# Kernel tuning notes

Measured on AMD Instinct MI355X. Metric: run time of the kernel, lower is better.

The kernel has to match this reference:

```python
import jax, jax.numpy as jnp
import numpy as np

S, DIM, H, HD, RATIO = 1024, 1024, 16, 64, 4
EH = H * RATIO  # expanded heads = 64


def setup_inputs() -> dict:
    key = jax.random.key(0)
    ks = jax.random.split(key, 9)
    sc = 0.02
    return {
        "x": jax.random.normal(ks[0], (S, DIM), jnp.float32),
        "qkv_w": jax.random.normal(ks[1], (3 * DIM, DIM), jnp.float32) * sc,
        "qkv_b": jnp.zeros((3 * DIM,), jnp.float32),
        "proj_w": jax.random.normal(ks[2], (DIM, DIM), jnp.float32) * sc,
        "proj_b": jnp.zeros((DIM,), jnp.float32),
        "ap1_w": jax.random.normal(ks[3], (EH, H), jnp.float32) * 0.25,
        "ap1_b": jnp.zeros((EH,), jnp.float32),
        "ap2_w": jax.random.normal(ks[4], (H, EH), jnp.float32) * 0.125,
        "ap2_b": jnp.zeros((H,), jnp.float32),
    }


def reference(x, qkv_w, qkv_b, proj_w, proj_b, ap1_w, ap1_b, ap2_w, ap2_b):
    # qkv projection: s, 3*dim -> (3, h, s, d)
    qkv = x @ qkv_w.T + qkv_b
    qkv = qkv.reshape(S, 3, H, HD).transpose(1, 2, 0, 3)
    q, k, v = qkv[0], qkv[1], qkv[2]  # each [h, s, d]

    # scaled QK^T scores [h, q, k]
    attn = jnp.einsum("hqd,hkd->hqk", q, k) / jnp.sqrt(jnp.float32(HD))

    # talking-heads pre-softmax mix over head axis: [h,q,k] -> [e,q,k]
    attn = jnp.einsum("hqk,eh->eqk", attn, ap1_w) + ap1_b[:, None, None]

    # softmax over key axis (original: softmax axis=1 on 'q k h' layout)
    attn = jax.nn.softmax(attn, axis=2)

    # talking-heads post-softmax mix back: [e,q,k] -> [h,q,k]
    attn = jnp.einsum("eqk,he->hqk", attn, ap2_w) + ap2_b[:, None, None]

    # attn @ V, merge heads, output projection
    out = jnp.einsum("hqk,hkd->hqd", attn, v)
    out = out.transpose(1, 0, 2).reshape(S, DIM)
    return out @ proj_w.T + proj_b
```

## Files before the change

### kernel.cpp

```cpp
#include <hip/hip_runtime.h>
#include <hip/hip_bf16.h>
#include <cstdint>

#define S_LEN 1024
#define DIM   1024
#define NH    16
#define HD    64
#define EH    64

typedef __attribute__((ext_vector_type(8))) short short8v;
typedef __attribute__((ext_vector_type(4))) float f32x4;

static __device__ __forceinline__ short f2bf(float f) {
  union { float f; uint32_t u; } v; v.f = f;
  const uint32_t r = v.u + 0x7FFF + ((v.u >> 16) & 1);
  return (short)(r >> 16);
}
static __device__ __forceinline__ uint32_t packbf(float a, float b) {
  return (uint32_t)(uint16_t)f2bf(a) | ((uint32_t)(uint16_t)f2bf(b) << 16);
}

__global__ __launch_bounds__(256) void prep(
    const float* __restrict__ x, const float* __restrict__ qw,
    const float* __restrict__ pw, const float* __restrict__ proj_b,
    short* __restrict__ xb, short* __restrict__ wqb, short* __restrict__ wpb,
    float* __restrict__ out)
{
  const int i = blockIdx.x * 256 + threadIdx.x;
  if (i < 655360) {
    const float* s; short* d; int j = i;
    if (j < 131072)       { s = x;  d = xb; }
    else if (j < 524288)  { j -= 131072; s = qw; d = wqb; }
    else                  { j -= 524288; s = pw; d = wpb; }
    const float4 a = ((const float4*)s)[2 * j];
    const float4 b = ((const float4*)s)[2 * j + 1];
    short8v o;
    o[0] = f2bf(a.x); o[1] = f2bf(a.y); o[2] = f2bf(a.z); o[3] = f2bf(a.w);
    o[4] = f2bf(b.x); o[5] = f2bf(b.y); o[6] = f2bf(b.z); o[7] = f2bf(b.w);
    *(short8v*)(d + 8 * (size_t)j) = o;
  } else {
    const int j = i - 655360;
    ((float4*)out)[j] = ((const float4*)proj_b)[j & 255];
  }
}

__global__ __launch_bounds__(256) void transpose_v(
    const short* __restrict__ qkvb, short* __restrict__ Vt)
{
  const int h  = blockIdx.y;
  const int k0 = blockIdx.x * 32;
  const int d  = threadIdx.x & 63;
  const int kw = threadIdx.x >> 6;
  const short* src = qkvb + 2048 + h * 64 + d;
  short8v o;
  #pragma unroll
  for (int j = 0; j < 8; ++j)
    o[j] = src[(size_t)(k0 + kw * 8 + j) * 3072];
  *(short8v*)(Vt + ((size_t)h * 64 + d) * 1024 + k0 + kw * 8) = o;
}

template<int BM, int NSPLIT, int CMODE>
__global__ __launch_bounds__(256) void gemm_v2(
    const short* __restrict__ A, int lda, long long aStride,
    const short* __restrict__ B, int ldb, long long bStride,
    void* __restrict__ C_, int ldc, long long cStride,
    int K, float alpha, const float* __restrict__ bias)
{
  constexpr int MS = BM / 32;
  __shared__ short As[BM * 64];
  __shared__ short Bs[64 * 64];

  const int z = blockIdx.z, batch = z / NSPLIT, split = z % NSPLIT;
  A += (size_t)batch * aStride;
  B += (size_t)batch * bStride;

  const int t = threadIdx.x, wid = t >> 6, lane = t & 63;
  const int wr = wid >> 1, wc = wid & 1;
  const int fr = lane & 15, kg = lane >> 4;
  const int m0 = blockIdx.y * BM, n0 = blockIdx.x * 64;
  const int klen = K / NSPLIT, kbeg = split * klen;

  f32x4 acc[MS][2] = {};

  for (int k0 = kbeg; k0 < kbeg + klen; k0 += 64) {
    #pragma unroll
    for (int i = 0; i < BM / 32; ++i) {
      const int p = t + i * 256;
      const int row = p >> 3, pc = p & 7;
      *(short8v*)&As[row * 64 + ((pc ^ (row & 7)) << 3)] =
          *(const short8v*)(A + (size_t)(m0 + row) * lda + k0 + pc * 8);
    }
    #pragma unroll
    for (int i = 0; i < 2; ++i) {
      const int p = t + i * 256;
      const int row = p >> 3, pc = p & 7;
      *(short8v*)&Bs[row * 64 + ((pc ^ (row & 7)) << 3)] =
          *(const short8v*)(B + (size_t)(n0 + row) * ldb + k0 + pc * 8);
    }
    __syncthreads();

    #pragma unroll
    for (int sub = 0; sub < 2; ++sub) {
      short8v af[MS], bg[2];
      #pragma unroll
      for (int ms = 0; ms < MS; ++ms) {
        const int row = wr * (BM / 2) + ms * 16 + fr;
        af[ms] = *(const short8v*)&As[row * 64 + (((sub * 4 + kg) ^ (row & 7)) << 3)];
      }
      #pragma unroll
      for (int ns = 0; ns < 2; ++ns) {
        const int row = wc * 32 + ns * 16 + fr;
        bg[ns] = *(const short8v*)&Bs[row * 64 + (((sub * 4 + kg) ^ (row & 7)) << 3)];
      }
      #pragma unroll
      for (int ms = 0; ms < MS; ++ms)
        #pragma unroll
        for (int ns = 0; ns < 2; ++ns)
          acc[ms][ns] = __builtin_amdgcn_mfma_f32_16x16x32_bf16(
              af[ms], bg[ns], acc[ms][ns], 0, 0, 0);
    }
    __syncthreads();
  }

  #pragma unroll
  for (int ms = 0; ms < MS; ++ms) {
    #pragma unroll
    for (int ns = 0; ns < 2; ++ns) {
      const int col = n0 + wc * 32 + ns * 16 + fr;
      const float bv = (CMODE == 0 && bias) ? bias[col] : 0.f;
      #pragma unroll
      for (int j = 0; j < 4; ++j) {
        const int row = m0 + wr * (BM / 2) + ms * 16 + kg * 4 + j;
        const float val = acc[ms][ns][j] * alpha + bv;
        const size_t off = (size_t)batch * cStride + (size_t)row * ldc + col;
        if constexpr (CMODE == 0) ((short*)C_)[off] = f2bf(val);
        else                      atomicAdd((float*)C_ + off, val);
      }
    }
  }
}

__global__ __launch_bounds__(256) void scores_direct(
    const short* __restrict__ qkvb, short* __restrict__ Sb)
{
  const int h = blockIdx.z;
  const int t = threadIdx.x, wid = t >> 6, lane = t & 63;
  const int wr = wid >> 1, wc = wid & 1;
  const int fr = lane & 15, kg = lane >> 4;
  const int m0 = blockIdx.y * 128, n0 = blockIdx.x * 64;

  const short* Aq = qkvb + h * 64;
  const short* Bk = qkvb + 1024 + h * 64;

  f32x4 acc[4][2] = {};
  #pragma unroll
  for (int sub = 0; sub < 2; ++sub) {
    const int d8 = (sub * 4 + kg) * 8;
    short8v af[4], bg[2];
    #pragma unroll
    for (int ms = 0; ms < 4; ++ms)
      af[ms] = *(const short8v*)(Aq + (size_t)(m0 + wr * 64 + ms * 16 + fr) * 3072 + d8);
    #pragma unroll
    for (int ns = 0; ns < 2; ++ns)
      bg[ns] = *(const short8v*)(Bk + (size_t)(n0 + wc * 32 + ns * 16 + fr) * 3072 + d8);
    #pragma unroll
    for (int ms = 0; ms < 4; ++ms)
      #pragma unroll
      for (int ns = 0; ns < 2; ++ns)
        acc[ms][ns] = __builtin_amdgcn_mfma_f32_16x16x32_bf16(
            af[ms], bg[ns], acc[ms][ns], 0, 0, 0);
  }

  short* Ch = Sb + ((size_t)h << 20);
  #pragma unroll
  for (int ms = 0; ms < 4; ++ms)
    #pragma unroll
    for (int ns = 0; ns < 2; ++ns) {
      const int col = n0 + wc * 32 + ns * 16 + fr;
      #pragma unroll
      for (int j = 0; j < 4; ++j) {
        const int row = m0 + wr * 64 + ms * 16 + kg * 4 + j;
        Ch[(size_t)row * 1024 + col] = f2bf(acc[ms][ns][j] * 0.125f);
      }
    }
}

__global__ __launch_bounds__(256, 3) void mix_softmax(
    short* __restrict__ Sb,
    const float* __restrict__ ap1_w,
    const float* __restrict__ ap2_w,
    const float* __restrict__ ap2_b)
{
  __shared__ short St[S_LEN][16];
  __shared__ short Pt[4][16][72];
  __shared__ float red[4][EH];
  __shared__ float il_tab[EH];

  const int q = blockIdx.x, t = threadIdx.x;
  const int w = t >> 6, lane = t & 63, kg = lane >> 4, fr = lane & 15;
  const size_t qoff = (size_t)q << 10;

  for (int i = t; i < 1024; i += 256) {
    const int hp = i & 7, k8 = (i >> 3) * 8;
    const short8v v0 = *(const short8v*)(Sb + ((size_t)(2 * hp)     << 20) + qoff + k8);
    const short8v v1 = *(const short8v*)(Sb + ((size_t)(2 * hp + 1) << 20) + qoff + k8);
    #pragma unroll
    for (int j = 0; j < 8; ++j) {
      const uint32_t u = (uint32_t)(uint16_t)v0[j] | ((uint32_t)(uint16_t)v1[j] << 16);
      *(uint32_t*)&St[k8 + j][2 * hp] = u;
    }
  }

  short8v af1[4];
  #pragma unroll
  for (int ms = 0; ms < 4; ++ms) {
    short8v v;
    #pragma unroll
    for (int j = 0; j < 8; ++j) v[j] = 0;
    if (kg < 2) {
      const int e = ms * 16 + fr;
      #pragma unroll
      for (int j = 0; j < 8; ++j) v[j] = f2bf(ap1_w[e * 16 + kg * 8 + j]);
    }
    af1[ms] = v;
  }
  float b2[4];
  #pragma unroll
  for (int j = 0; j < 4; ++j) b2[j] = ap2_b[kg * 4 + j];
  __syncthreads();

  const int kbase = w * 256;
  const f32x4 zc = {0.f, 0.f, 0.f, 0.f};

  float ls[4][4] = {};
  for (int s = 0; s < 16; ++s) {
    const int krow = kbase + s * 16 + fr;
    short8v bg;
    #pragma unroll
    for (int j = 0; j < 8; ++j) bg[j] = 0;
    if (kg < 2) bg = *(const short8v*)&St[krow][kg * 8];
    #pragma unroll
    for (int ms = 0; ms < 4; ++ms) {
      const f32x4 zv = __builtin_amdgcn_mfma_f32_16x16x32_bf16(af1[ms], bg, zc, 0, 0, 0);
      #pragma unroll
      for (int j = 0; j < 4; ++j) ls[ms][j] += __expf(zv[j]);
    }
  }
  #pragma unroll
  for (int ms = 0; ms < 4; ++ms)
    #pragma unroll
    for (int j = 0; j < 4; ++j) {
      float v = ls[ms][j];
      v += __shfl_xor(v, 1); v += __shfl_xor(v, 2);
      v += __shfl_xor(v, 4); v += __shfl_xor(v, 8);
      ls[ms][j] = v;
    }
  if (fr == 0)
    #pragma unroll
    for (int ms = 0; ms < 4; ++ms)
      #pragma unroll
      for (int j = 0; j < 4; ++j) red[w][ms * 16 + kg * 4 + j] = ls[ms][j];
  __syncthreads();
  if (t < EH)
    il_tab[t] = 1.f / (red[0][t] + red[1][t] + red[2][t] + red[3][t]);
  __syncthreads();

  short8v af2[2];
  #pragma unroll
  for (int half = 0; half < 2; ++half) {
    short8v v;
    #pragma unroll
    for (int j = 0; j < 8; ++j) {
      const int e = half * 32 + kg * 8 + j;
      v[j] = f2bf(ap2_w[fr * 64 + e] * il_tab[e]);
    }
    af2[half] = v;
  }

  for (int s = 0; s < 16; ++s) {
    const int krow = kbase + s * 16 + fr;
    short8v bg;
    #pragma unroll
    for (int j = 0; j < 8; ++j) bg[j] = 0;
    if (kg < 2) bg = *(const short8v*)&St[krow][kg * 8];
    #pragma unroll
    for (int ms = 0; ms < 4; ++ms) {
      const f32x4 zv = __builtin_amdgcn_mfma_f32_16x16x32_bf16(af1[ms], bg, zc, 0, 0, 0);
      const float p0 = __expf(zv[0]);
      const float p1 = __expf(zv[1]);
      const float p2 = __expf(zv[2]);
      const float p3 = __expf(zv[3]);
      *(uint32_t*)&Pt[w][fr][ms * 16 + kg * 4]     = packbf(p0, p1);
      *(uint32_t*)&Pt[w][fr][ms * 16 + kg * 4 + 2] = packbf(p2, p3);
    }
    f32x4 o = zc;
    const short8v pv0 = *(const short8v*)&Pt[w][fr][kg * 8];
    const short8v pv1 = *(const short8v*)&Pt[w][fr][32 + kg * 8];
    o = __builtin_amdgcn_mfma_f32_16x16x32_bf16(af2[0], pv0, o, 0, 0, 0);
    o = __builtin_amdgcn_mfma_f32_16x16x32_bf16(af2[1], pv1, o, 0, 0, 0);
    const int kcol = kbase + s * 16 + fr;
    #pragma unroll
    for (int j = 0; j < 4; ++j)
      Sb[((size_t)(kg * 4 + j) << 20) + qoff + kcol] = f2bf(o[j] + b2[j]);
  }
}

extern "C" void kernel_launch(void* const* d_in, const int* in_sizes, int n_in,
                              void* d_out, int out_size, void* d_ws, size_t ws_size,
                              hipStream_t stream)
{
  (void)in_sizes; (void)n_in; (void)out_size; (void)ws_size;

  const float* x      = (const float*)d_in[0];
  const float* qkv_w  = (const float*)d_in[1];
  const float* qkv_b  = (const float*)d_in[2];
  const float* proj_w = (const float*)d_in[3];
  const float* proj_b = (const float*)d_in[4];
  const float* ap1_w  = (const float*)d_in[5];
  const float* ap2_w  = (const float*)d_in[7];
  const float* ap2_b  = (const float*)d_in[8];
  float* out = (float*)d_out;

  short* xb    = (short*)d_ws;
  short* wqb   = xb   + (size_t)(1 << 20);
  short* wpb   = wqb  + (size_t)3 * (1 << 20);
  short* qkvb  = wpb  + (size_t)(1 << 20);
  short* Sb    = qkvb + (size_t)3 * (1 << 20);
  short* Vt    = Sb   + (size_t)16 * (1 << 20);
  short* attnb = xb;

  prep<<<dim3(3584), 256, 0, stream>>>(x, qkv_w, proj_w, proj_b,
                                       xb, wqb, wpb, out);

  gemm_v2<128, 1, 0><<<dim3(48, 8, 1), 256, 0, stream>>>(
      xb, DIM, 0, wqb, DIM, 0, qkvb, 3 * DIM, 0, DIM, 1.f, qkv_b);

  scores_direct<<<dim3(16, 8, NH), 256, 0, stream>>>(qkvb, Sb);

  transpose_v<<<dim3(32, NH), 256, 0, stream>>>(qkvb, Vt);

  mix_softmax<<<dim3(S_LEN), 256, 0, stream>>>(Sb, ap1_w, ap2_w, ap2_b);

  gemm_v2<64, 1, 0><<<dim3(1, 16, NH), 256, 0, stream>>>(
      Sb, S_LEN, (long long)S_LEN * S_LEN, Vt, S_LEN, (long long)HD * S_LEN,
      attnb, DIM, HD, S_LEN, 1.f, nullptr);

  gemm_v2<128, 2, 2><<<dim3(16, 8, 2), 256, 0, stream>>>(
      attnb, DIM, 0, wpb, DIM, 0, out, DIM, 0, DIM, 1.f, nullptr);
}
```

Baseline: 216.2 us.

## Fuse talking-heads mix/softmax with attn@V and stage epilogues via LDS

Replaces the mix_softmax kernel and the batched attn@V GEMM with one mix_av kernel. It processes 4 queries per block, recomputes the pre-softmax mix in two passes (log-sum-exp, then normalized probabilities), mixes back to 16 heads and multiplies by V^T in the same loop. This avoids writing the mixed attention back to the 32 MB score buffer and re-reading it. The ap2 bias is folded in through column sums of V, which transpose_v computes with atomics. GEMM and scores epilogues now stage through shared memory for coalesced 16-byte stores. The fused kernel launches only 256 blocks and streams V from global memory every chunk, so occupancy and V reuse may be limited.

```diff
diff --git a/kernel.cpp b/kernel.cpp
--- a/kernel.cpp
+++ b/kernel.cpp
@@ -7,6 +7,9 @@
 #define NH    16
 #define HD    64
 #define EH    64
+#define QB    4
+#define KC    64
+#define NCH   16
 
 typedef __attribute__((ext_vector_type(8))) short short8v;
 typedef __attribute__((ext_vector_type(4))) float f32x4;
@@ -16,6 +19,10 @@
   const uint32_t r = v.u + 0x7FFF + ((v.u >> 16) & 1);
   return (short)(r >> 16);
 }
+static __device__ __forceinline__ float bf2f(short s) {
+  union { uint32_t u; float f; } v; v.u = ((uint32_t)(uint16_t)s) << 16;
+  return v.f;
+}
 static __device__ __forceinline__ uint32_t packbf(float a, float b) {
   return (uint32_t)(uint16_t)f2bf(a) | ((uint32_t)(uint16_t)f2bf(b) << 16);
 }
@@ -24,7 +31,7 @@
     const float* __restrict__ x, const float* __restrict__ qw,
     const float* __restrict__ pw, const float* __restrict__ proj_b,
     short* __restrict__ xb, short* __restrict__ wqb, short* __restrict__ wpb,
-    float* __restrict__ out)
+    float* __restrict__ out, float* __restrict__ Vsum)
 {
   const int i = blockIdx.x * 256 + threadIdx.x;
   if (i < 655360) {
@@ -38,14 +45,17 @@
     o[0] = f2bf(a.x); o[1] = f2bf(a.y); o[2] = f2bf(a.z); o[3] = f2bf(a.w);
     o[4] = f2bf(b.x); o[5] = f2bf(b.y); o[6] = f2bf(b.z); o[7] = f2bf(b.w);
     *(short8v*)(d + 8 * (size_t)j) = o;
-  } else {
+  } else if (i < 917504) {
     const int j = i - 655360;
     ((float4*)out)[j] = ((const float4*)proj_b)[j & 255];
+  } else if (i < 918528) {
+    Vsum[i - 917504] = 0.f;
   }
 }
 
 __global__ __launch_bounds__(256) void transpose_v(
-    const short* __restrict__ qkvb, short* __restrict__ Vt)
+    const short* __restrict__ qkvb, short* __restrict__ Vt,
+    float* __restrict__ Vsum)
 {
   const int h  = blockIdx.y;
   const int k0 = blockIdx.x * 32;
@@ -53,22 +63,26 @@
   const int kw = threadIdx.x >> 6;
   const short* src = qkvb + 2048 + h * 64 + d;
   short8v o;
-  #pragma unroll
-  for (int j = 0; j < 8; ++j)
+  float s = 0.f;
+  #pragma unroll
+  for (int j = 0; j < 8; ++j) {
     o[j] = src[(size_t)(k0 + kw * 8 + j) * 3072];
+    s += bf2f(o[j]);
+  }
   *(short8v*)(Vt + ((size_t)h * 64 + d) * 1024 + k0 + kw * 8) = o;
-}
-
-template<int BM, int NSPLIT, int CMODE>
+  atomicAdd(&Vsum[h * 64 + d], s);
+}
+
+template<int NSPLIT, int CMODE>
 __global__ __launch_bounds__(256) void gemm_v2(
     const short* __restrict__ A, int lda, long long aStride,
     const short* __restrict__ B, int ldb, long long bStride,
     void* __restrict__ C_, int ldc, long long cStride,
     int K, float alpha, const float* __restrict__ bias)
 {
-  constexpr int MS = BM / 32;
-  __shared__ short As[BM * 64];
-  __shared__ short Bs[64 * 64];
+  __shared__ short sbuf[128 * 64 + 64 * 64];
+  short* As = sbuf;
+  short* Bs = sbuf + 128 * 64;
 
   const int z = blockIdx.z, batch = z / NSPLIT, split = z % NSPLIT;
   A += (size_t)batch * aStride;
@@ -77,14 +91,14 @@
   const int t = threadIdx.x, wid = t >> 6, lane = t & 63;
   const int wr = wid >> 1, wc = wid & 1;
   const int fr = lane & 15, kg = lane >> 4;
-  const int m0 = blockIdx.y * BM, n0 = blockIdx.x * 64;
+  const int m0 = blockIdx.y * 128, n0 = blockIdx.x * 64;
   const int klen = K / NSPLIT, kbeg = split * klen;
 
-  f32x4 acc[MS][2] = {};
+  f32x4 acc[4][2] = {};
 
   for (int k0 = kbeg; k0 < kbeg + klen; k0 += 64) {
     #pragma unroll
-    for (int i = 0; i < BM / 32; ++i) {
+    for (int i = 0; i < 4; ++i) {
       const int p = t + i * 256;
       const int row = p >> 3, pc = p & 7;
       *(short8v*)&As[row * 64 + ((pc ^ (row & 7)) << 3)] =
@@ -101,10 +115,10 @@
 
     #pragma unroll
     for (int sub = 0; sub < 2; ++sub) {
-      short8v af[MS], bg[2];
-      #pragma unroll
-      for (int ms = 0; ms < MS; ++ms) {
-        const int row = wr * (BM / 2) + ms * 16 + fr;
+      short8v af[4], bg[2];
+      #pragma unroll
+      for (int ms = 0; ms < 4; ++ms) {
+        const int row = wr * 64 + ms * 16 + fr;
         af[ms] = *(const short8v*)&As[row * 64 + (((sub * 4 + kg) ^ (row & 7)) << 3)];
       }
       #pragma unroll
@@ -113,7 +127,7 @@
         bg[ns] = *(const short8v*)&Bs[row * 64 + (((sub * 4 + kg) ^ (row & 7)) << 3)];
       }
       #pragma unroll
-      for (int ms = 0; ms < MS; ++ms)
+      for (int ms = 0; ms < 4; ++ms)
         #pragma unroll
         for (int ns = 0; ns < 2; ++ns)
           acc[ms][ns] = __builtin_amdgcn_mfma_f32_16x16x32_bf16(
@@ -122,27 +136,49 @@
     __syncthreads();
   }
 
-  #pragma unroll
-  for (int ms = 0; ms < MS; ++ms) {
-    #pragma unroll
-    for (int ns = 0; ns < 2; ++ns) {
-      const int col = n0 + wc * 32 + ns * 16 + fr;
-      const float bv = (CMODE == 0 && bias) ? bias[col] : 0.f;
-      #pragma unroll
-      for (int j = 0; j < 4; ++j) {
-        const int row = m0 + wr * (BM / 2) + ms * 16 + kg * 4 + j;
-        const float val = acc[ms][ns][j] * alpha + bv;
-        const size_t off = (size_t)batch * cStride + (size_t)row * ldc + col;
-        if constexpr (CMODE == 0) ((short*)C_)[off] = f2bf(val);
-        else                      atomicAdd((float*)C_ + off, val);
-      }
-    }
-  }
-}
-
-__global__ __launch_bounds__(256) void scores_direct(
+  if constexpr (CMODE == 0) {
+    short* Cb = sbuf;
+    #pragma unroll
+    for (int ms = 0; ms < 4; ++ms)
+      #pragma unroll
+      for (int ns = 0; ns < 2; ++ns) {
+        const int col = wc * 32 + ns * 16 + fr;
+        const float bv = bias ? bias[n0 + col] : 0.f;
+        #pragma unroll
+        for (int j = 0; j < 4; ++j) {
+          const int row = wr * 64 + ms * 16 + kg * 4 + j;
+          Cb[row * 72 + col] = f2bf(acc[ms][ns][j] * alpha + bv);
+        }
+      }
+    __syncthreads();
+    short* Cg = (short*)C_ + (size_t)batch * cStride;
+    #pragma unroll
+    for (int i = 0; i < 4; ++i) {
+      const int p = t + i * 256;
+      const int row = p >> 3, c8 = (p & 7) << 3;
+      *(short8v*)(Cg + (size_t)(m0 + row) * ldc + n0 + c8) =
+          *(const short8v*)&Cb[row * 72 + c8];
+    }
+  } else {
+    float* Cg = (float*)C_ + (size_t)batch * cStride;
+    #pragma unroll
+    for (int ms = 0; ms < 4; ++ms)
+      #pragma unroll
+      for (int ns = 0; ns < 2; ++ns) {
+        const int col = n0 + wc * 32 + ns * 16 + fr;
+        #pragma unroll
+        for (int j = 0; j < 4; ++j) {
+          const int row = m0 + wr * 64 + ms * 16 + kg * 4 + j;
+          atomicAdd(Cg + (size_t)row * ldc + col, acc[ms][ns][j] * alpha);
+        }
+      }
+  }
+}
+
+__global__ __launch_bounds__(256) void scores_v2(
     const short* __restrict__ qkvb, short* __restrict__ Sb)
 {
+  __shared__ short Cb[128][72];
   const int h = blockIdx.z;
   const int t = threadIdx.x, wid = t >> 6, lane = t & 63;
   const int wr = wid >> 1, wc = wid & 1;
@@ -171,45 +207,48 @@
             af[ms], bg[ns], acc[ms][ns], 0, 0, 0);
   }
 
+  #pragma unroll
+  for (int ms = 0; ms < 4; ++ms)
+    #pragma unroll
+    for (int ns = 0; ns < 2; ++ns) {
+      const int col = wc * 32 + ns * 16 + fr;
+      #pragma unroll
+      for (int j = 0; j < 4; ++j)
+        Cb[wr * 64 + ms * 16 + kg * 4 + j][col] = f2bf(acc[ms][ns][j] * 0.125f);
+    }
+  __syncthreads();
   short* Ch = Sb + ((size_t)h << 20);
   #pragma unroll
-  for (int ms = 0; ms < 4; ++ms)
-    #pragma unroll
-    for (int ns = 0; ns < 2; ++ns) {
-      const int col = n0 + wc * 32 + ns * 16 + fr;
-      #pragma unroll
-      for (int j = 0; j < 4; ++j) {
-        const int row = m0 + wr * 64 + ms * 16 + kg * 4 + j;
-        Ch[(size_t)row * 1024 + col] = f2bf(acc[ms][ns][j] * 0.125f);
-      }
-    }
-}
-
-__global__ __launch_bounds__(256, 3) void mix_softmax(
-    short* __restrict__ Sb,
-    const float* __restrict__ ap1_w,
-    const float* __restrict__ ap2_w,
-    const float* __restrict__ ap2_b)
-{
-  __shared__ short St[S_LEN][16];
-  __shared__ short Pt[4][16][72];
-  __shared__ float red[4][EH];
-  __shared__ float il_tab[EH];
-
-  const int q = blockIdx.x, t = threadIdx.x;
-  const int w = t >> 6, lane = t & 63, kg = lane >> 4, fr = lane & 15;
-  const size_t qoff = (size_t)q << 10;
-
-  for (int i = t; i < 1024; i += 256) {
-    const int hp = i & 7, k8 = (i >> 3) * 8;
-    const short8v v0 = *(const short8v*)(Sb + ((size_t)(2 * hp)     << 20) + qoff + k8);
-    const short8v v1 = *(const short8v*)(Sb + ((size_t)(2 * hp + 1) << 20) + qoff + k8);
-    #pragma unroll
-    for (int j = 0; j < 8; ++j) {
-      const uint32_t u = (uint32_t)(uint16_t)v0[j] | ((uint32_t)(uint16_t)v1[j] << 16);
-      *(uint32_t*)&St[k8 + j][2 * hp] = u;
-    }
-  }
+  for (int i = 0; i < 4; ++i) {
+    const int p = t + i * 256;
+    const int row = p >> 3, c8 = (p & 7) << 3;
+    *(short8v*)(Ch + (size_t)(m0 + row) * 1024 + n0 + c8) =
+        *(const short8v*)&Cb[row][c8];
+  }
+}
+
+__global__ __launch_bounds__(512) void mix_av(
+    const short* __restrict__ Sb, const short* __restrict__ Vt,
+    const float* __restrict__ ap1_w, const float* __restrict__ ap2_w,
+    const float* __restrict__ ap2_b, const float* __restrict__ Vsum,
+    short* __restrict__ attnb)
+{
+  __shared__ short St[QB * KC][24];
+  __shared__ short Pm[NH][QB][72];
+  __shared__ short Pt[8][16][72];
+  __shared__ float l_acc[2][EH][QB];
+  __shared__ short Ob[QB][1032];
+
+  const int t = threadIdx.x;
+  const int w = t >> 6, lane = t & 63;
+  const int kg = lane >> 4, fr = lane & 15;
+  const int qv = w & 3, half = w >> 2;
+  const int q0 = blockIdx.x * QB;
+
+  if (t < 2 * EH * QB) ((float*)l_acc)[t] = 0.f;
+
+  const int sh = t & 15, sq = (t >> 4) & 3, sk8 = (t >> 6) << 3;
+  const short* sp = Sb + ((size_t)sh << 20) + ((size_t)(q0 + sq) << 10);
 
   short8v af1[4];
   #pragma unroll
@@ -224,84 +263,146 @@
     }
     af1[ms] = v;
   }
-  float b2[4];
-  #pragma unroll
-  for (int j = 0; j < 4; ++j) b2[j] = ap2_b[kg * 4 + j];
-  __syncthreads();
-
-  const int kbase = w * 256;
+  short8v af2[2];
+  #pragma unroll
+  for (int half2 = 0; half2 < 2; ++half2) {
+    short8v v;
+    #pragma unroll
+    for (int j = 0; j < 8; ++j)
+      v[j] = f2bf(ap2_w[fr * 64 + half2 * 32 + kg * 8 + j]);
+    af2[half2] = v;
+  }
+
   const f32x4 zc = {0.f, 0.f, 0.f, 0.f};
 
-  float ls[4][4] = {};
-  for (int s = 0; s < 16; ++s) {
-    const int krow = kbase + s * 16 + fr;
-    short8v bg;
-    #pragma unroll
-    for (int j = 0; j < 8; ++j) bg[j] = 0;
-    if (kg < 2) bg = *(const short8v*)&St[krow][kg * 8];
-    #pragma unroll
-    for (int ms = 0; ms < 4; ++ms) {
-      const f32x4 zv = __builtin_amdgcn_mfma_f32_16x16x32_bf16(af1[ms], bg, zc, 0, 0, 0);
-      #pragma unroll
-      for (int j = 0; j < 4; ++j) ls[ms][j] += __expf(zv[j]);
+  float l16[4][4] = {};
+  for (int c = 0; c < NCH; ++c) {
+    const short8v v = *(const short8v*)(sp + c * KC + sk8);
+    __syncthreads();
+    #pragma unroll
+    for (int j = 0; j < 8; ++j) St[sq * 64 + sk8 + j][sh] = v[j];
+    __syncthreads();
+    #pragma unroll
+    for (int tt = 0; tt < 2; ++tt) {
+      const int tile = 4 * qv + 2 * half + tt;
+      short8v bg;
+      #pragma unroll
+      for (int j = 0; j < 8; ++j) bg[j] = 0;
+      if (kg < 2) bg = *(const short8v*)&St[tile * 16 + fr][kg * 8];
+      #pragma unroll
+      for (int ms = 0; ms < 4; ++ms) {
+        const f32x4 zv = __builtin_amdgcn_mfma_f32_16x16x32_bf16(af1[ms], bg, zc, 0, 0, 0);
+        #pragma unroll
+        for (int j = 0; j < 4; ++j) l16[ms][j] += __expf(zv[j]);
+      }
     }
   }
   #pragma unroll
   for (int ms = 0; ms < 4; ++ms)
     #pragma unroll
     for (int j = 0; j < 4; ++j) {
-      float v = ls[ms][j];
+      float v = l16[ms][j];
       v += __shfl_xor(v, 1); v += __shfl_xor(v, 2);
       v += __shfl_xor(v, 4); v += __shfl_xor(v, 8);
-      ls[ms][j] = v;
-    }
+      l16[ms][j] = v;
+    }
+  __syncthreads();
   if (fr == 0)
     #pragma unroll
     for (int ms = 0; ms < 4; ++ms)
       #pragma unroll
-      for (int j = 0; j < 4; ++j) red[w][ms * 16 + kg * 4 + j] = ls[ms][j];
-  __syncthreads();
-  if (t < EH)
-    il_tab[t] = 1.f / (red[0][t] + red[1][t] + red[2][t] + red[3][t]);
-  __syncthreads();
-
-  short8v af2[2];
-  #pragma unroll
-  for (int half = 0; half < 2; ++half) {
-    short8v v;
-    #pragma unroll
-    for (int j = 0; j < 8; ++j) {
-      const int e = half * 32 + kg * 8 + j;
-      v[j] = f2bf(ap2_w[fr * 64 + e] * il_tab[e]);
-    }
-    af2[half] = v;
-  }
-
-  for (int s = 0; s < 16; ++s) {
-    const int krow = kbase + s * 16 + fr;
-    short8v bg;
-    #pragma unroll
-    for (int j = 0; j < 8; ++j) bg[j] = 0;
-    if (kg < 2) bg = *(const short8v*)&St[krow][kg * 8];
-    #pragma unroll
-    for (int ms = 0; ms < 4; ++ms) {
-      const f32x4 zv = __builtin_amdgcn_mfma_f32_16x16x32_bf16(af1[ms], bg, zc, 0, 0, 0);
-      const float p0 = __expf(zv[0]);
-      const float p1 = __expf(zv[1]);
-      const float p2 = __expf(zv[2]);
-      const float p3 = __expf(zv[3]);
-      *(uint32_t*)&Pt[w][fr][ms * 16 + kg * 4]     = packbf(p0, p1);
-      *(uint32_t*)&Pt[w][fr][ms * 16 + kg * 4 + 2] = packbf(p2, p3);
-    }
-    f32x4 o = zc;
-    const short8v pv0 = *(const short8v*)&Pt[w][fr][kg * 8];
-    const short8v pv1 = *(const short8v*)&Pt[w][fr][32 + kg * 8];
-    o = __builtin_amdgcn_mfma_f32_16x16x32_bf16(af2[0], pv0, o, 0, 0, 0);
-    o = __builtin_amdgcn_mfma_f32_16x16x32_bf16(af2[1], pv1, o, 0, 0, 0);
-    const int kcol = kbase + s * 16 + fr;
+      for (int j = 0; j < 4; ++j)
+        l_acc[half][ms * 16 + kg * 4 + j][qv] = l16[ms][j];
+  __syncthreads();
+  if (t < 256) {
+    const int e = t >> 2, q = t & 3;
+    l_acc[0][e][q] = logf(l_acc[0][e][q] + l_acc[1][e][q]);
+  }
+  __syncthreads();
+  float Lreg[4][4];
+  #pragma unroll
+  for (int ms = 0; ms < 4; ++ms)
     #pragma unroll
     for (int j = 0; j < 4; ++j)
-      Sb[((size_t)(kg * 4 + j) << 20) + qoff + kcol] = f2bf(o[j] + b2[j]);
+      Lreg[ms][j] = l_acc[0][ms * 16 + kg * 4 + j][qv];
+
+  f32x4 avacc[2][4] = {};
+  const int h0 = w * 2;
+  for (int c = 0; c < NCH; ++c) {
+    const short8v v = *(const short8v*)(sp + c * KC + sk8);
+    __syncthreads();
+    #pragma unroll
+    for (int j = 0; j < 8; ++j) St[sq * 64 + sk8 + j][sh] = v[j];
+    __syncthreads();
+    #pragma unroll
+    for (int tt = 0; tt < 2; ++tt) {
+      const int tile = 4 * qv + 2 * half + tt;
+      short8v bg;
+      #pragma unroll
+      for (int j = 0; j < 8; ++j) bg[j] = 0;
+      if (kg < 2) bg = *(const short8v*)&St[tile * 16 + fr][kg * 8];
+      #pragma unroll
+      for (int ms = 0; ms < 4; ++ms) {
+        const f32x4 zv = __builtin_amdgcn_mfma_f32_16x16x32_bf16(af1[ms], bg, zc, 0, 0, 0);
+        const float p0 = __expf(zv[0] - Lreg[ms][0]);
+        const float p1 = __expf(zv[1] - Lreg[ms][1]);
+        const float p2 = __expf(zv[2] - Lreg[ms][2]);
+        const float p3 = __expf(zv[3] - Lreg[ms][3]);
+        *(uint32_t*)&Pt[w][fr][ms * 16 + kg * 4]     = packbf(p0, p1);
+        *(uint32_t*)&Pt[w][fr][ms * 16 + kg * 4 + 2] = packbf(p2, p3);
+      }
+      f32x4 o = zc;
+      const short8v pv0 = *(const short8v*)&Pt[w][fr][kg * 8];
+      const short8v pv1 = *(const short8v*)&Pt[w][fr][32 + kg * 8];
+      o = __builtin_amdgcn_mfma_f32_16x16x32_bf16(af2[0], pv0, o, 0, 0, 0);
+      o = __builtin_amdgcn_mfma_f32_16x16x32_bf16(af2[1], pv1, o, 0, 0, 0);
+      const int kk = (2 * half + tt) * 16 + fr;
+      #pragma unroll
+      for (int jj = 0; jj < 4; ++jj)
+        Pm[kg * 4 + jj][qv][kk] = f2bf(o[jj]);
+    }
+    __syncthreads();
+    #pragma unroll
+    for (int hh = 0; hh < 2; ++hh) {
+      const int h = h0 + hh;
+      #pragma unroll
+      for (int chain = 0; chain < 2; ++chain) {
+        short8v pa;
+        #pragma unroll
+        for (int j = 0; j < 8; ++j) pa[j] = 0;
+        if (fr < QB) pa = *(const short8v*)&Pm[h][fr][chain * 32 + kg * 8];
+        #pragma unroll
+        for (int dblk = 0; dblk < 4; ++dblk) {
+          const short8v vb = *(const short8v*)(
+              Vt + ((size_t)h * 64 + dblk * 16 + fr) * 1024 + c * KC + chain * 32 + kg * 8);
+          avacc[hh][dblk] = __builtin_amdgcn_mfma_f32_16x16x32_bf16(
+              pa, vb, avacc[hh][dblk], 0, 0, 0);
+        }
+      }
+    }
+  }
+
+  __syncthreads();
+  #pragma unroll
+  for (int hh = 0; hh < 2; ++hh) {
+    const int h = h0 + hh;
+    const float b2 = ap2_b[h];
+    #pragma unroll
+    for (int dblk = 0; dblk < 4; ++dblk) {
+      if (kg == 0) {
+        const int d = dblk * 16 + fr;
+        const float vs = Vsum[h * 64 + d];
+        #pragma unroll
+        for (int j = 0; j < 4; ++j)
+          Ob[j][h * 64 + d] = f2bf(avacc[hh][dblk][j] + b2 * vs);
+      }
+    }
+  }
+  __syncthreads();
+  {
+    const int row = t >> 7, c8 = (t & 127) << 3;
+    *(short8v*)(attnb + ((size_t)(q0 + row) << 10) + c8) =
+        *(const short8v*)&Ob[row][c8];
   }
 }
 
@@ -327,24 +428,21 @@
   short* qkvb  = wpb  + (size_t)(1 << 20);
   short* Sb    = qkvb + (size_t)3 * (1 << 20);
   short* Vt    = Sb   + (size_t)16 * (1 << 20);
+  float* Vsum  = (float*)(Vt + (size_t)(1 << 20));
   short* attnb = xb;
 
-  prep<<<dim3(3584), 256, 0, stream>>>(x, qkv_w, proj_w, proj_b,
-                                       xb, wqb, wpb, out);
-
-  gemm_v2<128, 1, 0><<<dim3(48, 8, 1), 256, 0, stream>>>(
+  prep<<<dim3(3588), 256, 0, stream>>>(x, qkv_w, proj_w, proj_b,
+                                       xb, wqb, wpb, out, Vsum);
+
+  gemm_v2<1, 0><<<dim3(48, 8, 1), 256, 0, stream>>>(
       xb, DIM, 0, wqb, DIM, 0, qkvb, 3 * DIM, 0, DIM, 1.f, qkv_b);
 
-  scores_direct<<<dim3(16, 8, NH), 256, 0, stream>>>(qkvb, Sb);
-
-  transpose_v<<<dim3(32, NH), 256, 0, stream>>>(qkvb, Vt);
-
-  mix_softmax<<<dim3(S_LEN), 256, 0, stream>>>(Sb, ap1_w, ap2_w, ap2_b);
-
-  gemm_v2<64, 1, 0><<<dim3(1, 16, NH), 256, 0, stream>>>(
-      Sb, S_LEN, (long long)S_LEN * S_LEN, Vt, S_LEN, (long long)HD * S_LEN,
-      attnb, DIM, HD, S_LEN, 1.f, nullptr);
-
-  gemm_v2<128, 2, 2><<<dim3(16, 8, 2), 256, 0, stream>>>(
+  scores_v2<<<dim3(16, 8, NH), 256, 0, stream>>>(qkvb, Sb);
+
+  transpose_v<<<dim3(32, NH), 256, 0, stream>>>(qkvb, Vt, Vsum);
+
+  mix_av<<<dim3(256), 512, 0, stream>>>(Sb, Vt, ap1_w, ap2_w, ap2_b, Vsum, attnb);
+
+  gemm_v2<2, 2><<<dim3(16, 8, 2), 256, 0, stream>>>(
       attnb, DIM, 0, wpb, DIM, 0, out, DIM, 0, DIM, 1.f, nullptr);
 }
```

After: 242.0 us. 11.9% more time.
